# Optimization experiments

Hardware: AMD Instinct MI355X
Metric: run time of the kernel (lower is better)

## Reference

```python
import jax, jax.numpy as jnp
import numpy as np
import math

B, L, D = 4, 4096, 512
P, V = 128, 8  # n_phases, value_dim
PI = math.pi

def _lin(x, w, b):
    return x @ w + b

def _gelu(x):
    return jax.nn.gelu(x, approximate=False)  # torch default exact GELU

def setup_inputs() -> dict:
    key = jax.random.key(0)
    ks = iter(jax.random.split(key, 32))
    def rn(shape, scale=0.02):
        return (jax.random.normal(next(ks), shape, dtype=jnp.float32) * scale)
    inp = {
        'x': jax.random.normal(next(ks), (B, L, D), dtype=jnp.float32),
        'pos_phases': jax.random.normal(next(ks), (L, D), dtype=jnp.float32) * PI,
        'magnitude_scale': jnp.float32(5.0),
        'w_v': rn((D, D)), 'b_v': jnp.zeros((D,), jnp.float32),
        'w_o': rn((D, D)), 'b_o': jnp.zeros((D,), jnp.float32),
        'w_m': rn((D, D)), 'b_m': jnp.zeros((D,), jnp.float32),
        'w_q': rn((D, D)), 'b_q': jnp.zeros((D,), jnp.float32),
        'w_ke': rn((D, P)), 'b_ke': jnp.zeros((P,), jnp.float32),
        'w_ve': rn((D, V)), 'b_ve': jnp.zeros((V,), jnp.float32),
        'w_s1': rn((2 * D, D)), 'b_s1': jnp.zeros((D,), jnp.float32),
        'w_s2': rn((D, P)), 'b_s2': jnp.zeros((P,), jnp.float32),
        'w_g': rn((D, 1)), 'b_g': jnp.zeros((1,), jnp.float32),
        'w_kv': rn((V, D)), 'b_kv': jnp.zeros((D,), jnp.float32),
        'ln_g': jnp.ones((2 * D,), jnp.float32), 'ln_b': jnp.zeros((2 * D,), jnp.float32),
        'w_t1': rn((2 * D, 2 * D)), 'b_t1': jnp.zeros((2 * D,), jnp.float32),
        'w_t2': rn((2 * D, D)), 'b_t2': jnp.zeros((D,), jnp.float32),
    }
    return inp

def _forward(x, pos_phases, magnitude_scale, w_v, b_v, w_o, b_o, w_m, b_m,
             w_q, b_q, w_ke, b_ke, w_ve, b_ve, w_s1, b_s1, w_s2, b_s2,
             w_g, b_g, w_kv, b_kv, ln_g, ln_b, w_t1, b_t1, w_t2, b_t2):
    b, l, d = x.shape
    phi = pos_phases[:l]                               # [L,D]
    cos_phi, sin_phi = jnp.cos(phi), jnp.sin(phi)
    # --- positional phasor memory ---
    v1 = _lin(x, w_v, b_v)                             # [B,L,D]
    magnitude = jax.nn.sigmoid(_lin(x, w_m, b_m)) * jnp.abs(magnitude_scale)
    weighted_v1 = magnitude * v1
    mem1_cos = jnp.cumsum(weighted_v1 * cos_phi, axis=1)
    mem1_sin = jnp.cumsum(weighted_v1 * sin_phi, axis=1)
    sqrt_mag = jnp.sqrt(jnp.cumsum(magnitude, axis=1) + 1e-8)
    mem1_cos = mem1_cos / sqrt_mag
    mem1_sin = mem1_sin / sqrt_mag
    phi_query = phi + _lin(x, w_q, b_q)
    pos_ret = (mem1_cos * jnp.cos(phi_query) + mem1_sin * jnp.sin(phi_query)) / math.sqrt(d)
    pos_out = _lin(pos_ret, w_o, b_o)                  # [B,L,D]
    # --- key-value phasor memory ---
    query_phase = jnp.tanh(_lin(x, w_ke, b_ke)) * PI   # [B,L,P]
    values = _lin(x, w_ve, b_ve)                       # [B,L,V]
    store_gate = jax.nn.sigmoid(_lin(x, w_g, b_g))     # [B,L,1]
    positions = jnp.arange(1, l + 1, dtype=x.dtype)[None, :, None]
    context_avg = jnp.cumsum(x, axis=1) / positions
    sk = _lin(_gelu(_lin(jnp.concatenate([x, context_avg], axis=-1), w_s1, b_s1)), w_s2, b_s2)
    storage_phase = jnp.tanh(sk) * PI                  # [B,L,P]
    gv = values * store_gate                           # [B,L,V]
    kv_bound_cos = jnp.cos(storage_phase)[..., None] * gv[:, :, None, :]  # [B,L,P,V]
    kv_bound_sin = jnp.sin(storage_phase)[..., None] * gv[:, :, None, :]
    kv_mem_cos = jnp.cumsum(kv_bound_cos, axis=1)
    kv_mem_sin = jnp.cumsum(kv_bound_sin, axis=1)
    gate_cumsum = jnp.clip(jnp.cumsum(store_gate, axis=1), 1.0, None)     # [B,L,1]
    inv = 1.0 / jnp.sqrt(gate_cumsum)[..., None]
    kv_mem_cos = kv_mem_cos * inv
    kv_mem_sin = kv_mem_sin * inv
    kv_retrieved = (jnp.cos(query_phase)[..., None] * kv_mem_cos
                    + jnp.sin(query_phase)[..., None] * kv_mem_sin).sum(axis=2) / math.sqrt(P)
    kv_out = _lin(kv_retrieved, w_kv, b_kv)            # [B,L,D]
    # --- output projection (dropout = eval/identity) ---
    combined = jnp.concatenate([pos_out, kv_out], axis=-1)  # [B,L,2D]
    mu = combined.mean(axis=-1, keepdims=True)
    var = combined.var(axis=-1, keepdims=True)
    ln = (combined - mu) / jnp.sqrt(var + 1e-5) * ln_g + ln_b
    return x + _lin(_gelu(_lin(ln, w_t1, b_t1)), w_t2, b_t2)

def reference(x, pos_phases, magnitude_scale, w_v, b_v, w_o, b_o, w_m, b_m,
              w_q, b_q, w_ke, b_ke, w_ve, b_ve, w_s1, b_s1, w_s2, b_s2,
              w_g, b_g, w_kv, b_kv, ln_g, ln_b, w_t1, b_t1, w_t2, b_t2):
    return _forward(x, pos_phases, magnitude_scale, w_v, b_v, w_o, b_o, w_m, b_m,
                    w_q, b_q, w_ke, b_ke, w_ve, b_ve, w_s1, b_s1, w_s2, b_s2,
                    w_g, b_g, w_kv, b_kv, ln_g, ln_b, w_t1, b_t1, w_t2, b_t2)
```

## Files before the change

### kernel.cpp

```cpp
#include <hip/hip_runtime.h>
#include <math.h>

#define NTOK 16384
#define LSEQ 4096
#define BATCH 4
#define DDIM 512
#define PDIM 128
#define VDIM 8
#define PI_F 3.14159265358979323846f

#define NC2 64
#define CL2 64
#define NC3 128
#define CL3 32

#define VMQ_S 1536

typedef __attribute__((ext_vector_type(8))) short bfrag8;
typedef __attribute__((ext_vector_type(4))) float facc4;

__device__ __forceinline__ float sigmoid_(float v) { return 1.0f / (1.0f + expf(-v)); }
__device__ __forceinline__ float gelu_(float v) { return 0.5f * v * (1.0f + erff(v * 0.70710678118654752f)); }

__device__ __forceinline__ unsigned short f2bf(float f) {
    unsigned int u = __builtin_bit_cast(unsigned int, f);
    u += 0x7fffu + ((u >> 16) & 1u);
    return (unsigned short)(u >> 16);
}
__device__ __forceinline__ float bf2f(unsigned short h) {
    return __builtin_bit_cast(float, ((unsigned int)h) << 16);
}
__device__ __forceinline__ float bflo(unsigned int w) { return __builtin_bit_cast(float, w << 16); }
__device__ __forceinline__ float bfhi(unsigned int w) { return __builtin_bit_cast(float, w & 0xffff0000u); }

__device__ __forceinline__ void async16(const unsigned short* g, unsigned short* l) {
    __builtin_amdgcn_global_load_lds(
        (const __attribute__((address_space(1))) unsigned int*)g,
        (__attribute__((address_space(3))) unsigned int*)l, 16, 0, 0);
}

__global__ __launch_bounds__(256) void gemm_bf16(
    const unsigned short* __restrict__ A, int ldA,
    const unsigned short* __restrict__ Wt,
    const float* __restrict__ bias, int K,
    float* __restrict__ Cf, unsigned short* __restrict__ Cb, int ldC, int colOff,
    const float* __restrict__ res, int ldRes,
    int act)
{
    __shared__ unsigned short Asm[3][128 * 32];
    __shared__ unsigned short Bsm[3][128 * 32];
    const int tid = threadIdx.x;
    const int lane = tid & 63;
    const int wv = tid >> 6;
    const int wm = wv & 1, wn = wv >> 1;
    const int quad = lane >> 4, cc = lane & 15;

    const int C = gridDim.x, R = gridDim.y;
    const int bid = blockIdx.x + C * blockIdx.y;
    const int xcd = bid & 7;
    const int s = bid >> 3;
    const int by = xcd * (R >> 3) + s / C;
    const int bx = s - (s / C) * C;
    const int row0 = by << 7;
    const int col0 = bx << 7;

    facc4 acc[4][4];
#pragma unroll
    for (int i = 0; i < 4; ++i)
#pragma unroll
        for (int j = 0; j < 4; ++j) acc[i][j] = (facc4){0.f, 0.f, 0.f, 0.f};

    const int rquad = tid >> 2;
    const int kq = tid & 3;

    const unsigned short* ga0 = A + (size_t)(row0 + rquad) * ldA + kq * 8;
    const unsigned short* ga1 = ga0 + (size_t)64 * ldA;
    const unsigned short* gb0 = Wt + (size_t)(col0 + rquad) * K + kq * 8;
    const unsigned short* gb1 = gb0 + (size_t)64 * K;

    const int nk = K >> 5;

    auto stage = [&](int t, int buf) {
        const int off = t << 5;
        async16(ga0 + off, &Asm[buf][tid * 8]);
        async16(ga1 + off, &Asm[buf][(256 + tid) * 8]);
        async16(gb0 + off, &Bsm[buf][tid * 8]);
        async16(gb1 + off, &Bsm[buf][(256 + tid) * 8]);
    };

    stage(0, 0);
    stage(1, 1);

    int cur = 0;
    for (int t = 0; t < nk; ++t) {
        int nb = cur + 2; if (nb >= 3) nb -= 3;
        if (t + 2 < nk) stage(t + 2, nb);
        if (t + 2 < nk)      asm volatile("s_waitcnt vmcnt(8)" ::: "memory");
        else if (t + 1 < nk) asm volatile("s_waitcnt vmcnt(4)" ::: "memory");
        else                 asm volatile("s_waitcnt vmcnt(0)" ::: "memory");
        __builtin_amdgcn_s_barrier();
        __builtin_amdgcn_sched_barrier(0);
        bfrag8 afr[4], bfr[4];
#pragma unroll
        for (int mt = 0; mt < 4; ++mt)
            afr[mt] = *(const bfrag8*)&Asm[cur][(wm * 64 + mt * 16 + cc) * 32 + quad * 8];
#pragma unroll
        for (int nt = 0; nt < 4; ++nt)
            bfr[nt] = *(const bfrag8*)&Bsm[cur][(wn * 64 + nt * 16 + cc) * 32 + quad * 8];
#pragma unroll
        for (int mt = 0; mt < 4; ++mt)
#pragma unroll
            for (int nt = 0; nt < 4; ++nt)
                acc[mt][nt] = __builtin_amdgcn_mfma_f32_16x16x32_bf16(
                    afr[mt], bfr[nt], acc[mt][nt], 0, 0, 0);
        asm volatile("s_waitcnt lgkmcnt(0)" ::: "memory");
        __builtin_amdgcn_s_barrier();
        cur = cur + 1; if (cur >= 3) cur -= 3;
    }

#pragma unroll
    for (int nt = 0; nt < 4; ++nt) {
        int col = col0 + wn * 64 + nt * 16 + cc;
        float bvv = bias[col];
#pragma unroll
        for (int mt = 0; mt < 4; ++mt) {
            int rowb = row0 + wm * 64 + mt * 16 + quad * 4;
#pragma unroll
            for (int r = 0; r < 4; ++r) {
                float v = acc[mt][nt][r] + bvv;
                if (act == 1) v = gelu_(v);
                size_t row = (size_t)(rowb + r);
                if (res) v += res[row * ldRes + col];
                size_t idx = row * ldC + colOff + col;
                if (Cf) Cf[idx] = v;
                else    Cb[idx] = f2bf(v);
            }
        }
    }
}

__global__ __launch_bounds__(256) void k_wcvt(const float* __restrict__ W, int K, int N,
                                              unsigned short* __restrict__ Wt)
{
    __shared__ float t[32][33];
    int bx = blockIdx.x, by = blockIdx.y;
    int tid = threadIdx.x;
    int tx = tid & 31, ty = tid >> 5;
#pragma unroll
    for (int r = 0; r < 4; ++r) {
        int k = by * 32 + ty + r * 8;
        t[ty + r * 8][tx] = W[(size_t)k * N + bx * 32 + tx];
    }
    __syncthreads();
#pragma unroll
    for (int r = 0; r < 4; ++r) {
        int n = bx * 32 + ty + r * 8;
        Wt[(size_t)n * K + by * 32 + tx] = f2bf(t[tx][ty + r * 8]);
    }
}

__global__ void k_xcvt(const float* __restrict__ x, unsigned short* __restrict__ xcat)
{
    int g = blockIdx.x * 256 + threadIdx.x;
    int c = g & 511, r = g >> 9;
    xcat[(size_t)r * 1024 + c] = f2bf(x[g]);
}

__global__ void k_bpack(const float* __restrict__ b0, const float* __restrict__ b1,
                        const float* __restrict__ b2, float* __restrict__ dst)
{
    int i = blockIdx.x * 256 + threadIdx.x;
    if (i < 512) dst[i] = b0[i];
    else if (i < 1024) dst[i] = b1[i - 512];
    else if (i < 1536) dst[i] = b2[i - 1024];
}

__global__ void k_phi(const float* __restrict__ pp, float* __restrict__ cphi,
                      float* __restrict__ sphi, int n)
{
    int i = blockIdx.x * 256 + threadIdx.x;
    if (i < n) {
        float s, c;
        sincosf(pp[i], &s, &c);
        cphi[i] = c;
        sphi[i] = s;
    }
}

__global__ __launch_bounds__(256) void k_glin(const float* __restrict__ x,
                                              const float* __restrict__ wg,
                                              const float* __restrict__ bg,
                                              float* __restrict__ glin)
{
    int wid = threadIdx.x >> 6, lane = threadIdx.x & 63;
    int row = blockIdx.x * 4 + wid;
    const float4* xr = (const float4*)(x + (size_t)row * DDIM);
    const float4* w4 = (const float4*)wg;
    float4 a0 = xr[lane], a1 = xr[lane + 64];
    float4 w0 = w4[lane], w1 = w4[lane + 64];
    float p = a0.x * w0.x + a0.y * w0.y + a0.z * w0.z + a0.w * w0.w
            + a1.x * w1.x + a1.y * w1.y + a1.z * w1.z + a1.w * w1.w;
    for (int d = 32; d >= 1; d >>= 1) p += __shfl_down(p, d, 64);
    if (lane == 0) glin[row] = p + bg[0];
}

__global__ __launch_bounds__(256) void k_values(const float* __restrict__ x,
                                                const float* __restrict__ wve,
                                                const float* __restrict__ bve,
                                                const float* __restrict__ glin,
                                                float* __restrict__ gv)
{
    int g = blockIdx.x * 256 + threadIdx.x;
    int m = g & 7, r = g >> 3;
    const float4* xr = (const float4*)(x + (size_t)r * DDIM);
    float acc = bve[m];
    for (int kq = 0; kq < 128; ++kq) {
        float4 a = xr[kq];
        int k = kq * 4;
        acc += a.x * wve[k * 8 + m] + a.y * wve[(k + 1) * 8 + m]
             + a.z * wve[(k + 2) * 8 + m] + a.w * wve[(k + 3) * 8 + m];
    }
    gv[g] = acc * sigmoid_(glin[r]);
}

__global__ __launch_bounds__(256) void k_scan1a(
    const unsigned short* __restrict__ vmq, const float* __restrict__ x,
    const float* __restrict__ cphi, const float* __restrict__ sphi,
    const float* __restrict__ msp, float* __restrict__ sum2)
{
    int g = blockIdx.x * 256 + threadIdx.x;
    int d = g & 511;
    int rest = g >> 9;
    int chunk = rest & (NC2 - 1);
    int b = rest >> 6;
    float msabs = fabsf(msp[0]);
    size_t row = (size_t)b * LSEQ + chunk * CL2;
    const unsigned short* vp = vmq + row * VMQ_S + d;
    const float* xp = x + row * DDIM + d;
    size_t pbase = ((size_t)chunk * CL2) * DDIM + d;
    float ac = 0.f, as = 0.f, am = 0.f, ax = 0.f;
    for (int i = 0; i < CL2; ++i) {
        float vv = bf2f(vp[0]);
        float ml = bf2f(vp[512]);
        float xv = xp[0];
        float cp = cphi[pbase], sp = sphi[pbase];
        float mag = msabs * sigmoid_(ml);
        float wv = mag * vv;
        ac += wv * cp; as += wv * sp; am += mag; ax += xv;
        vp += VMQ_S; xp += DDIM; pbase += DDIM;
    }
    int col = (b * DDIM + d) * NC2 + chunk;
    sum2[0 * 131072 + col] = ac;
    sum2[1 * 131072 + col] = as;
    sum2[2 * 131072 + col] = am;
    sum2[3 * 131072 + col] = ax;
}

__global__ __launch_bounds__(256) void k_scan1b(float* __restrict__ sum2)
{
    int g = blockIdx.x * 256 + threadIdx.x;
    float* p = sum2 + (size_t)g * NC2;
    float run = 0.f;
    for (int i = 0; i < NC2; ++i) { float t = p[i]; p[i] = run; run += t; }
}

__global__ __launch_bounds__(256) void k_scan1c(
    const unsigned short* __restrict__ vmq, const float* __restrict__ x,
    const float* __restrict__ cphi, const float* __restrict__ sphi,
    const float* __restrict__ msp, const float* __restrict__ sum2,
    unsigned short* __restrict__ pret, unsigned short* __restrict__ xcat)
{
    int g = blockIdx.x * 256 + threadIdx.x;
    int d = g & 511;
    int rest = g >> 9;
    int chunk = rest & (NC2 - 1);
    int b = rest >> 6;
    float msabs = fabsf(msp[0]);
    int col = (b * DDIM + d) * NC2 + chunk;
    float ac = sum2[col];
    float as = sum2[131072 + col];
    float am = sum2[2 * 131072 + col];
    float ax = sum2[3 * 131072 + col];
    size_t row = (size_t)b * LSEQ + chunk * CL2;
    const unsigned short* vp = vmq + row * VMQ_S + d;
    size_t base = row * DDIM + d;
    size_t pbase = ((size_t)chunk * CL2) * DDIM + d;
    int l = chunk * CL2;
    const float rsd = 0.04419417382415922f;
    for (int i = 0; i < CL2; ++i, ++l) {
        float vv = bf2f(vp[0]);
        float ml = bf2f(vp[512]);
        float q = bf2f(vp[1024]);
        float xv = x[base];
        float cp = cphi[pbase], sp = sphi[pbase];
        float mag = msabs * sigmoid_(ml);
        float wv = mag * vv;
        ac += wv * cp; as += wv * sp; am += mag; ax += xv;
        float inv = rsqrtf(am + 1e-8f);
        float mc = ac * inv, msn = as * inv;
        float cq, sq;
        sincosf(q, &sq, &cq);
        float cpq = cp * cq - sp * sq;
        float spq = sp * cq + cp * sq;
        pret[base] = f2bf((mc * cpq + msn * spq) * rsd);
        size_t orow = (size_t)b * LSEQ + l;
        xcat[orow * 1024 + 512 + d] = f2bf(ax / (float)(l + 1));
        vp += VMQ_S; base += DDIM; pbase += DDIM;
    }
}

__global__ void k_phases(const float* __restrict__ sk, const unsigned short* __restrict__ ke,
                         unsigned short* __restrict__ csp, unsigned short* __restrict__ ssp,
                         unsigned short* __restrict__ cqp, unsigned short* __restrict__ sqp, int n)
{
    int g = blockIdx.x * 256 + threadIdx.x;
    if (g < n) {
        float s, c;
        float spv = tanhf(sk[g]) * PI_F;
        sincosf(spv, &s, &c);
        csp[g] = f2bf(c); ssp[g] = f2bf(s);
        float qpv = tanhf(bf2f(ke[g])) * PI_F;
        sincosf(qpv, &s, &c);
        cqp[g] = f2bf(c); sqp[g] = f2bf(s);
    }
}

__global__ __launch_bounds__(1024) void k_gatescan(const float* __restrict__ glin,
                                                   float* __restrict__ gcum)
{
    __shared__ float s[1024];
    int b = blockIdx.x, tid = threadIdx.x;
    const float* gp = glin + (size_t)b * LSEQ + tid * 4;
    float e0 = sigmoid_(gp[0]);
    float e1 = sigmoid_(gp[1]);
    float e2 = sigmoid_(gp[2]);
    float e3 = sigmoid_(gp[3]);
    float l0 = e0, l1 = l0 + e1, l2 = l1 + e2, l3 = l2 + e3;
    s[tid] = l3;
    __syncthreads();
    for (int off = 1; off < 1024; off <<= 1) {
        float t = (tid >= off) ? s[tid - off] : 0.0f;
        __syncthreads();
        s[tid] += t;
        __syncthreads();
    }
    float excl = s[tid] - l3;
    float* out = gcum + (size_t)b * LSEQ + tid * 4;
    out[0] = excl + l0; out[1] = excl + l1; out[2] = excl + l2; out[3] = excl + l3;
}

__device__ __forceinline__ size_t kv_sum_idx(int b, int p, int v) {
    return ((((size_t)b * PDIM + p) * VDIM + v) * 2) * NC3;
}

__global__ __launch_bounds__(256) void k_kv1(const unsigned short* __restrict__ csp,
                                             const unsigned short* __restrict__ ssp,
                                             const float* __restrict__ gv,
                                             float* __restrict__ sum3)
{
    int blk = blockIdx.x;
    int chunk = blk & (NC3 - 1), b = blk >> 7;
    int tid = threadIdx.x;
    int w = tid >> 6, lane = tid & 63;
    int v = 2 * w + (lane & 1);
    int pq = lane >> 1;
    float sc[4] = {0, 0, 0, 0}, ss[4] = {0, 0, 0, 0};
    const uint2* c2p = (const uint2*)csp;
    const uint2* s2p = (const uint2*)ssp;
    int t = b * LSEQ + chunk * CL3;
    for (int i = 0; i < CL3; ++i, ++t) {
        uint2 cu = c2p[(size_t)t * 32 + pq];
        uint2 su = s2p[(size_t)t * 32 + pq];
        float g = gv[(size_t)t * VDIM + v];
        sc[0] += bflo(cu.x) * g; sc[1] += bfhi(cu.x) * g;
        sc[2] += bflo(cu.y) * g; sc[3] += bfhi(cu.y) * g;
        ss[0] += bflo(su.x) * g; ss[1] += bfhi(su.x) * g;
        ss[2] += bflo(su.y) * g; ss[3] += bfhi(su.y) * g;
    }
#pragma unroll
    for (int j = 0; j < 4; ++j) {
        size_t base = kv_sum_idx(b, pq * 4 + j, v) + chunk;
        sum3[base] = sc[j];
        sum3[base + NC3] = ss[j];
    }
}

__global__ __launch_bounds__(256) void k_kv2(float* __restrict__ sum3)
{
    int g = blockIdx.x * 256 + threadIdx.x;
    float* p = sum3 + (size_t)g * NC3;
    float run = 0.f;
    for (int i = 0; i < NC3; ++i) { float t = p[i]; p[i] = run; run += t; }
}

__global__ __launch_bounds__(256) void k_kv3(const unsigned short* __restrict__ csp,
                                             const unsigned short* __restrict__ ssp,
                                             const unsigned short* __restrict__ cqp,
                                             const unsigned short* __restrict__ sqp,
                                             const float* __restrict__ gv,
                                             const float* __restrict__ gcum,
                                             const float* __restrict__ sum3,
                                             float* __restrict__ kvr)
{
    int blk = blockIdx.x;
    int chunk = blk & (NC3 - 1), b = blk >> 7;
    int tid = threadIdx.x;
    int w = tid >> 6, lane = tid & 63;
    int v = 2 * w + (lane & 1);
    int pq = lane >> 1;
    float sc[4], ss[4];
#pragma unroll
    for (int j = 0; j < 4; ++j) {
        size_t base = kv_sum_idx(b, pq * 4 + j, v) + chunk;
        sc[j] = sum3[base];
        ss[j] = sum3[base + NC3];
    }
    const uint2* c2p = (const uint2*)csp;
    const uint2* s2p = (const uint2*)ssp;
    const uint2* cq2p = (const uint2*)cqp;
    const uint2* sq2p = (const uint2*)sqp;
    const float rsp = 0.08838834764831845f;
    int t = b * LSEQ + chunk * CL3;
    for (int i = 0; i < CL3; ++i, ++t) {
        uint2 cu = c2p[(size_t)t * 32 + pq];
        uint2 su = s2p[(size_t)t * 32 + pq];
        float g = gv[(size_t)t * VDIM + v];
        sc[0] += bflo(cu.x) * g; sc[1] += bfhi(cu.x) * g;
        sc[2] += bflo(cu.y) * g; sc[3] += bfhi(cu.y) * g;
        ss[0] += bflo(su.x) * g; ss[1] += bfhi(su.x) * g;
        ss[2] += bflo(su.y) * g; ss[3] += bfhi(su.y) * g;
        uint2 qcu = cq2p[(size_t)t * 32 + pq];
        uint2 qsu = sq2p[(size_t)t * 32 + pq];
        float part = bflo(qcu.x) * sc[0] + bfhi(qcu.x) * sc[1]
                   + bflo(qcu.y) * sc[2] + bfhi(qcu.y) * sc[3]
                   + bflo(qsu.x) * ss[0] + bfhi(qsu.x) * ss[1]
                   + bflo(qsu.y) * ss[2] + bfhi(qsu.y) * ss[3];
        part += __shfl_down(part, 32, 64);
        part += __shfl_down(part, 16, 64);
        part += __shfl_down(part, 8, 64);
        part += __shfl_down(part, 4, 64);
        part += __shfl_down(part, 2, 64);
        if (lane < 2) {
            float gc = gcum[t];
            float scale = rsqrtf(fmaxf(gc, 1.0f)) * rsp;
            kvr[(size_t)t * VDIM + v] = part * scale;
        }
    }
}

__global__ __launch_bounds__(256) void k_kvout(const float* __restrict__ kvr,
                                               const float* __restrict__ wkv,
                                               const float* __restrict__ bkv,
                                               unsigned short* __restrict__ comb)
{
    int g = blockIdx.x * 256 + threadIdx.x;
    int c = g & 511, r = g >> 9;
    const float* kr = kvr + (size_t)r * VDIM;
    float acc = bkv[c];
#pragma unroll
    for (int k = 0; k < 8; ++k) acc += kr[k] * wkv[k * DDIM + c];
    comb[(size_t)r * 1024 + 512 + c] = f2bf(acc);
}

__global__ __launch_bounds__(256) void k_ln(unsigned short* __restrict__ comb,
                                            const float* __restrict__ gam,
                                            const float* __restrict__ bet)
{
    int wid = threadIdx.x >> 6, lane = threadIdx.x & 63;
    int row = blockIdx.x * 4 + wid;
    unsigned int* rp = (unsigned int*)(comb + (size_t)row * 1024);
    uint4 u0 = *(uint4*)&rp[lane * 8];
    uint4 u1 = *(uint4*)&rp[lane * 8 + 4];
    unsigned int uu[8] = {u0.x, u0.y, u0.z, u0.w, u1.x, u1.y, u1.z, u1.w};
    float v[16];
    float s = 0.f, s2 = 0.f;
#pragma unroll
    for (int j = 0; j < 8; ++j) {
        v[2 * j] = bflo(uu[j]);
        v[2 * j + 1] = bfhi(uu[j]);
        s += v[2 * j] + v[2 * j + 1];
        s2 += v[2 * j] * v[2 * j] + v[2 * j + 1] * v[2 * j + 1];
    }
    for (int m = 32; m >= 1; m >>= 1) {
        s += __shfl_xor(s, m, 64);
        s2 += __shfl_xor(s2, m, 64);
    }
    float mu = s * (1.0f / 1024.0f);
    float var = s2 * (1.0f / 1024.0f) - mu * mu;
    float inv = rsqrtf(var + 1e-5f);
    int c0 = lane * 16;
    unsigned int ou[8];
#pragma unroll
    for (int j = 0; j < 8; ++j) {
        float g0 = gam[c0 + 2 * j], g1 = gam[c0 + 2 * j + 1];
        float b0 = bet[c0 + 2 * j], b1 = bet[c0 + 2 * j + 1];
        float o0 = (v[2 * j] - mu) * inv * g0 + b0;
        float o1 = (v[2 * j + 1] - mu) * inv * g1 + b1;
        ou[j] = (unsigned int)f2bf(o0) | ((unsigned int)f2bf(o1) << 16);
    }
    *(uint4*)&rp[lane * 8] = make_uint4(ou[0], ou[1], ou[2], ou[3]);
    *(uint4*)&rp[lane * 8 + 4] = make_uint4(ou[4], ou[5], ou[6], ou[7]);
}

extern "C" void kernel_launch(void* const* d_in, const int* in_sizes, int n_in,
                              void* d_out, int out_size, void* d_ws, size_t ws_size,
                              hipStream_t stream)
{
    const float* x    = (const float*)d_in[0];
    const float* pp   = (const float*)d_in[1];
    const float* msp  = (const float*)d_in[2];
    const float* w_v  = (const float*)d_in[3];
    const float* b_v  = (const float*)d_in[4];
    const float* w_o  = (const float*)d_in[5];
    const float* b_o  = (const float*)d_in[6];
    const float* w_m  = (const float*)d_in[7];
    const float* b_m  = (const float*)d_in[8];
    const float* w_q  = (const float*)d_in[9];
    const float* b_q  = (const float*)d_in[10];
    const float* w_ke = (const float*)d_in[11];
    const float* b_ke = (const float*)d_in[12];
    const float* w_ve = (const float*)d_in[13];
    const float* b_ve = (const float*)d_in[14];
    const float* w_s1 = (const float*)d_in[15];
    const float* b_s1 = (const float*)d_in[16];
    const float* w_s2 = (const float*)d_in[17];
    const float* b_s2 = (const float*)d_in[18];
    const float* w_g  = (const float*)d_in[19];
    const float* b_g  = (const float*)d_in[20];
    const float* w_kv = (const float*)d_in[21];
    const float* b_kv = (const float*)d_in[22];
    const float* ln_g = (const float*)d_in[23];
    const float* ln_b = (const float*)d_in[24];
    const float* w_t1 = (const float*)d_in[25];
    const float* b_t1 = (const float*)d_in[26];
    const float* w_t2 = (const float*)d_in[27];
    const float* b_t2 = (const float*)d_in[28];
    float* out = (float*)d_out;
    float* ws = (float*)d_ws;
    (void)ws_size; (void)n_in; (void)in_sizes; (void)out_size;

    unsigned short* VMQ    = (unsigned short*)(ws);
    float*          SKf    = ws + 4194304;
    unsigned short* CSP    = (unsigned short*)(ws + 8388608);
    unsigned short* SSP    = CSP + 2097152;
    unsigned short* CQP    = CSP + 2 * 2097152;
    unsigned short* SQP    = CSP + 3 * 2097152;
    unsigned short* KEbf   = (unsigned short*)(ws + 12582912);
    float* GVb   = ws + 13631488;
    float* GLINb = ws + 13762560;
    float* GCUMb = ws + 13778944;
    float* SUM2b = ws + 13795328;
    float* CBIAS = SUM2b;
    float* SUM3b = ws + 14319616;
    float* KVRb  = ws + 15368192;
    float* CPHIb = ws + 15499264;
    float* SPHIb = ws + 17596416;
    unsigned short* HSbf   = (unsigned short*)(ws + 15499264);
    unsigned short* PRETbf = (unsigned short*)(ws + 19693568);
    unsigned short* XCAT   = (unsigned short*)(ws + 23887872);
    unsigned short* COMBbf = XCAT;
    unsigned short* HTbf   = (unsigned short*)(ws);
    unsigned short* WT     = (unsigned short*)(ws + 32276480);
    unsigned short* wv_t  = WT;
    unsigned short* wm_t  = WT + 262144;
    unsigned short* wq_t  = WT + 524288;
    unsigned short* wo_t  = WT + 786432;
    unsigned short* wke_t = WT + 1048576;
    unsigned short* ws1_t = WT + 1114112;
    unsigned short* ws2_t = WT + 1638400;
    unsigned short* wt1_t = WT + 1703936;
    unsigned short* wt2_t = WT + 2752512;

    k_phi<<<8192, 256, 0, stream>>>(pp, CPHIb, SPHIb, 2097152);
    k_xcvt<<<32768, 256, 0, stream>>>(x, XCAT);
    k_wcvt<<<dim3(16, 16), 256, 0, stream>>>(w_v, 512, 512, wv_t);
    k_wcvt<<<dim3(16, 16), 256, 0, stream>>>(w_m, 512, 512, wm_t);
    k_wcvt<<<dim3(16, 16), 256, 0, stream>>>(w_q, 512, 512, wq_t);
    k_wcvt<<<dim3(16, 16), 256, 0, stream>>>(w_o, 512, 512, wo_t);
    k_wcvt<<<dim3(4, 16), 256, 0, stream>>>(w_ke, 512, 128, wke_t);
    k_wcvt<<<dim3(16, 32), 256, 0, stream>>>(w_s1, 1024, 512, ws1_t);
    k_wcvt<<<dim3(4, 16), 256, 0, stream>>>(w_s2, 512, 128, ws2_t);
    k_wcvt<<<dim3(32, 32), 256, 0, stream>>>(w_t1, 1024, 1024, wt1_t);
    k_wcvt<<<dim3(16, 32), 256, 0, stream>>>(w_t2, 1024, 512, wt2_t);
    k_bpack<<<6, 256, 0, stream>>>(b_v, b_m, b_q, CBIAS);

    gemm_bf16<<<dim3(12, 128), 256, 0, stream>>>(XCAT, 1024, wv_t, CBIAS, 512, nullptr, VMQ, VMQ_S, 0, nullptr, 0, 0);
    gemm_bf16<<<dim3(1, 128), 256, 0, stream>>>(XCAT, 1024, wke_t, b_ke, 512, nullptr, KEbf, 128, 0, nullptr, 0, 0);
    k_glin<<<4096, 256, 0, stream>>>(x, w_g, b_g, GLINb);
    k_values<<<512, 256, 0, stream>>>(x, w_ve, b_ve, GLINb, GVb);

    k_scan1a<<<512, 256, 0, stream>>>(VMQ, x, CPHIb, SPHIb, msp, SUM2b);
    k_scan1b<<<32, 256, 0, stream>>>(SUM2b);
    k_scan1c<<<512, 256, 0, stream>>>(VMQ, x, CPHIb, SPHIb, msp, SUM2b, PRETbf, XCAT);

    gemm_bf16<<<dim3(4, 128), 256, 0, stream>>>(XCAT, 1024, ws1_t, b_s1, 1024, nullptr, HSbf, 512, 0, nullptr, 0, 1);
    gemm_bf16<<<dim3(1, 128), 256, 0, stream>>>(HSbf, 512, ws2_t, b_s2, 512, SKf, nullptr, 128, 0, nullptr, 0, 0);

    k_phases<<<8192, 256, 0, stream>>>(SKf, KEbf, CSP, SSP, CQP, SQP, 2097152);
    k_gatescan<<<4, 1024, 0, stream>>>(GLINb, GCUMb);

    k_kv1<<<512, 256, 0, stream>>>(CSP, SSP, GVb, SUM3b);
    k_kv2<<<32, 256, 0, stream>>>(SUM3b);
    k_kv3<<<512, 256, 0, stream>>>(CSP, SSP, CQP, SQP, GVb, GCUMb, SUM3b, KVRb);

    gemm_bf16<<<dim3(4, 128), 256, 0, stream>>>(PRETbf, 512, wo_t, b_o, 512, nullptr, COMBbf, 1024, 0, nullptr, 0, 0);
    k_kvout<<<32768, 256, 0, stream>>>(KVRb, w_kv, b_kv, COMBbf);
    k_ln<<<4096, 256, 0, stream>>>(COMBbf, ln_g, ln_b);
    gemm_bf16<<<dim3(8, 128), 256, 0, stream>>>(COMBbf, 1024, wt1_t, b_t1, 1024, nullptr, HTbf, 1024, 0, nullptr, 0, 1);
    gemm_bf16<<<dim3(4, 128), 256, 0, stream>>>(HTbf, 1024, wt2_t, b_t2, 1024, out, nullptr, 512, 0, x, 512, 0);
}
```

Before: 623.6 us.

## Use BK=64 double-buffered GEMM tiles with XOR-swizzled LDS layout

```diff
diff --git a/kernel.cpp b/kernel.cpp
--- a/kernel.cpp
+++ b/kernel.cpp
@@ -47,8 +47,8 @@
     const float* __restrict__ res, int ldRes,
     int act)
 {
-    __shared__ unsigned short Asm[3][128 * 32];
-    __shared__ unsigned short Bsm[3][128 * 32];
+    __shared__ unsigned short Asm[2][128 * 64];
+    __shared__ unsigned short Bsm[2][128 * 64];
     const int tid = threadIdx.x;
     const int lane = tid & 63;
     const int wv = tid >> 6;
@@ -70,52 +70,60 @@
 #pragma unroll
         for (int j = 0; j < 4; ++j) acc[i][j] = (facc4){0.f, 0.f, 0.f, 0.f};
 
-    const int rquad = tid >> 2;
-    const int kq = tid & 3;
-
-    const unsigned short* ga0 = A + (size_t)(row0 + rquad) * ldA + kq * 8;
-    const unsigned short* ga1 = ga0 + (size_t)64 * ldA;
-    const unsigned short* gb0 = Wt + (size_t)(col0 + rquad) * K + kq * 8;
-    const unsigned short* gb1 = gb0 + (size_t)64 * K;
-
-    const int nk = K >> 5;
+    const int nk = K >> 6;
+
+    int srow[4]; int soff[4]; int sdst[4];
+#pragma unroll
+    for (int k = 0; k < 4; ++k) {
+        int g = tid + k * 256;
+        int r = g >> 3, sd = g & 7;
+        srow[k] = r;
+        soff[k] = (sd ^ (r & 7)) * 8;
+        sdst[k] = g * 8;
+    }
 
     auto stage = [&](int t, int buf) {
-        const int off = t << 5;
-        async16(ga0 + off, &Asm[buf][tid * 8]);
-        async16(ga1 + off, &Asm[buf][(256 + tid) * 8]);
-        async16(gb0 + off, &Bsm[buf][tid * 8]);
-        async16(gb1 + off, &Bsm[buf][(256 + tid) * 8]);
+        const int koff = t << 6;
+#pragma unroll
+        for (int k = 0; k < 4; ++k) {
+            async16(A  + (size_t)(row0 + srow[k]) * ldA + koff + soff[k], &Asm[buf][sdst[k]]);
+            async16(Wt + (size_t)(col0 + srow[k]) * K   + koff + soff[k], &Bsm[buf][sdst[k]]);
+        }
     };
 
     stage(0, 0);
-    stage(1, 1);
-
+
+    const int swz = cc & 7;
     int cur = 0;
     for (int t = 0; t < nk; ++t) {
-        int nb = cur + 2; if (nb >= 3) nb -= 3;
-        if (t + 2 < nk) stage(t + 2, nb);
-        if (t + 2 < nk)      asm volatile("s_waitcnt vmcnt(8)" ::: "memory");
-        else if (t + 1 < nk) asm volatile("s_waitcnt vmcnt(4)" ::: "memory");
-        else                 asm volatile("s_waitcnt vmcnt(0)" ::: "memory");
+        if (t + 1 < nk) {
+            stage(t + 1, cur ^ 1);
+            asm volatile("s_waitcnt vmcnt(8)" ::: "memory");
+        } else {
+            asm volatile("s_waitcnt vmcnt(0)" ::: "memory");
+        }
         __builtin_amdgcn_s_barrier();
         __builtin_amdgcn_sched_barrier(0);
-        bfrag8 afr[4], bfr[4];
-#pragma unroll
-        for (int mt = 0; mt < 4; ++mt)
-            afr[mt] = *(const bfrag8*)&Asm[cur][(wm * 64 + mt * 16 + cc) * 32 + quad * 8];
-#pragma unroll
-        for (int nt = 0; nt < 4; ++nt)
-            bfr[nt] = *(const bfrag8*)&Bsm[cur][(wn * 64 + nt * 16 + cc) * 32 + quad * 8];
-#pragma unroll
-        for (int mt = 0; mt < 4; ++mt)
+#pragma unroll
+        for (int kk = 0; kk < 2; ++kk) {
+            const int sl = ((kk * 4 + quad) ^ swz) * 8;
+            bfrag8 afr[4], bfr[4];
+#pragma unroll
+            for (int mt = 0; mt < 4; ++mt)
+                afr[mt] = *(const bfrag8*)&Asm[cur][(wm * 64 + mt * 16 + cc) * 64 + sl];
 #pragma unroll
             for (int nt = 0; nt < 4; ++nt)
-                acc[mt][nt] = __builtin_amdgcn_mfma_f32_16x16x32_bf16(
-                    afr[mt], bfr[nt], acc[mt][nt], 0, 0, 0);
+                bfr[nt] = *(const bfrag8*)&Bsm[cur][(wn * 64 + nt * 16 + cc) * 64 + sl];
+#pragma unroll
+            for (int mt = 0; mt < 4; ++mt)
+#pragma unroll
+                for (int nt = 0; nt < 4; ++nt)
+                    acc[mt][nt] = __builtin_amdgcn_mfma_f32_16x16x32_bf16(
+                        afr[mt], bfr[nt], acc[mt][nt], 0, 0, 0);
+        }
         asm volatile("s_waitcnt lgkmcnt(0)" ::: "memory");
         __builtin_amdgcn_s_barrier();
-        cur = cur + 1; if (cur >= 3) cur -= 3;
+        cur ^= 1;
     }
 
 #pragma unroll
```

Result: faster. 593.6 us (-4.8%).
